# Kernel optimization log

Measured on AMD Instinct MI355X. Metric: run time of the kernel, lower is better.

The kernel has to match this reference:

```python
import jax, jax.numpy as jnp
import numpy as np

N_NODES, N_EDGES = 100000, 1600000
D_IN, D_H, D_OUT = 256, 128, 32


def _gcn_conv(x, W, b, row, col, norm, n):
    # GCNConv: transform, normalized gather from source nodes, scatter-sum at targets, bias.
    h = x @ W                                   # [n, d_out]
    msgs = h[row] * norm[:, None]               # [E', d_out] edge messages
    out = jax.ops.segment_sum(msgs, col, num_segments=n)
    return out + b


def setup_inputs() -> dict:
    key = jax.random.key(0)
    k = jax.random.split(key, 6)
    x = jax.random.normal(k[0], (N_NODES, D_IN), dtype=jnp.float32)
    edge_index = jax.random.randint(k[1], (2, N_EDGES), 0, N_NODES, dtype=jnp.int64)
    # Glorot-ish scaled params (GCNConv lin has no bias; bias added post-aggregation)
    W1 = jax.random.normal(k[2], (D_IN, D_H), dtype=jnp.float32) * (1.0 / np.sqrt(D_IN))
    b1 = jnp.zeros((D_H,), dtype=jnp.float32)
    W2 = jax.random.normal(k[3], (D_H, D_OUT), dtype=jnp.float32) * (1.0 / np.sqrt(D_H))
    b2 = jnp.zeros((D_OUT,), dtype=jnp.float32)
    return {"x": x, "W1": W1, "b1": b1, "W2": W2, "b2": b2, "edge_index": edge_index}


def reference(x, W1, b1, W2, b2, edge_index):
    n = x.shape[0]
    loops = jnp.arange(n, dtype=edge_index.dtype)
    row = jnp.concatenate([edge_index[0], loops])   # sources (incl. self-loops)
    col = jnp.concatenate([edge_index[1], loops])   # targets
    # symmetric normalization deg^{-1/2} (deg >= 1 because of self-loops)
    deg = jax.ops.segment_sum(jnp.ones_like(col, dtype=x.dtype), col, num_segments=n)
    dinv = deg ** -0.5
    norm = dinv[row] * dinv[col]
    h = jax.nn.relu(_gcn_conv(x, W1, b1, row, col, norm, n))
    # F.dropout(training=False) is identity in eval mode
    out = _gcn_conv(h, W2, b2, row, col, norm, n)
    return jax.nn.log_softmax(out, axis=1)
```

## Files before the change

kernel.cpp:

```cpp
#include <hip/hip_runtime.h>
#include <math.h>

#define N_NODES 100000
#define N_EDGES 1600000
#define D_IN 256
#define D_H 128
#define D_OUT 32
#define N_PAD 102400
#define NB 196
#define CAPB 10240
#define CHUNK 4096

typedef long long ll;
typedef unsigned int uint;
typedef unsigned short ushort;
typedef unsigned char uchar;
typedef short frag_ab __attribute__((ext_vector_type(8)));
typedef float frag_cd __attribute__((ext_vector_type(4)));

__device__ __forceinline__ ushort f2bf(float f) {
    uint u = __float_as_uint(f);
    u += 0x7FFFu + ((u >> 16) & 1u);
    return (ushort)(u >> 16);
}
__device__ __forceinline__ float bfl(uint u) { return __uint_as_float(u << 16); }
__device__ __forceinline__ float bfh(uint u) { return __uint_as_float(u & 0xFFFF0000u); }
__device__ __forceinline__ uint packbf(float a, float b) {
    return (uint)f2bf(a) | ((uint)f2bf(b) << 16);
}

__global__ __launch_bounds__(256) void k_prep(const float* __restrict__ W1,
                                              const float* __restrict__ W2,
                                              ushort* __restrict__ w1t,
                                              ushort* __restrict__ w2t,
                                              int* __restrict__ gcur) {
    int gi = blockIdx.x * 256 + threadIdx.x;
    if (blockIdx.x == 0) gcur[threadIdx.x] = 0;
    if (gi < D_IN * D_H) {
        int k = gi >> 7, nn = gi & 127;
        w1t[nn * D_IN + k] = f2bf(W1[gi]);
    } else if (gi < D_IN * D_H + D_H * D_OUT) {
        int j = gi - D_IN * D_H;
        int k = j >> 5, nn = j & 31;
        w2t[nn * D_H + k] = f2bf(W2[j]);
    }
}

__global__ __launch_bounds__(256, 3) void k_fused(const int* __restrict__ row,
                                                  const int* __restrict__ col,
                                                  int* __restrict__ gcur,
                                                  uint* __restrict__ pairs,
                                                  const float* __restrict__ x,
                                                  const ushort* __restrict__ w1t,
                                                  ushort* __restrict__ hxs,
                                                  int n, int e) {
    __shared__ int cnt[NB];
    __shared__ int cur[NB];
    __shared__ int lstart[NB];
    const int t = threadIdx.x;
    const int GA = (e + CHUNK - 1) / CHUNK;
    const int bid = blockIdx.x;

    if (bid < GA) {
        if (t < NB) { cnt[t] = 0; cur[t] = 0; }
        __syncthreads();
        const int base = bid * CHUNK;
        const int end = min(base + CHUNK, e);
        int rs[16], cs[16];
#pragma unroll
        for (int j = 0; j < 16; j++) {
            int idx = base + t + j * 256;
            bool ok = idx < end;
            int c = ok ? col[idx] : 0;
            rs[j] = ok ? row[idx] : 0;
            cs[j] = ok ? c : -1;
            if (ok) atomicAdd(&cnt[c >> 9], 1);
        }
        __syncthreads();
        if (t < NB) {
            int v = cnt[t];
            lstart[t] = (v > 0) ? atomicAdd(&gcur[t], v) : 0;
        }
        __syncthreads();
#pragma unroll
        for (int j = 0; j < 16; j++) {
            int c = cs[j];
            if (c >= 0) {
                int b = c >> 9;
                int pos = lstart[b] + atomicAdd(&cur[b], 1);
                if (pos < CAPB)
                    pairs[b * CAPB + pos] = ((uint)rs[j] << 9) | (uint)(c & 511);
            }
        }
    } else {
        const int id = bid - GA;
        const int wv = t >> 6, lane = t & 63;
        const int lm = lane & 15, quad = lane >> 4;
        const int base = id * 128 + wv * 32;

        frag_cd acc[2][8];
#pragma unroll
        for (int mt = 0; mt < 2; mt++)
#pragma unroll
            for (int nt = 0; nt < 8; nt++) acc[mt][nt] = (frag_cd){0.f, 0.f, 0.f, 0.f};

        const float4* xr[2];
#pragma unroll
        for (int mt = 0; mt < 2; mt++) {
            int node = base + mt * 16 + lm;
            xr[mt] = (const float4*)(x + (ll)min(node, n - 1) * D_IN);
        }

#pragma unroll
        for (int ks = 0; ks < 8; ks++) {
            frag_ab a[2];
#pragma unroll
            for (int mt = 0; mt < 2; mt++) {
                float4 v0 = xr[mt][ks * 8 + quad * 2];
                float4 v1 = xr[mt][ks * 8 + quad * 2 + 1];
                uint* ap = (uint*)&a[mt];
                ap[0] = packbf(v0.x, v0.y);
                ap[1] = packbf(v0.z, v0.w);
                ap[2] = packbf(v1.x, v1.y);
                ap[3] = packbf(v1.z, v1.w);
            }
#pragma unroll
            for (int nt = 0; nt < 8; nt++) {
                frag_ab b = *(const frag_ab*)&w1t[(nt * 16 + lm) * D_IN + ks * 32 + quad * 8];
#pragma unroll
                for (int mt = 0; mt < 2; mt++)
                    acc[mt][nt] = __builtin_amdgcn_mfma_f32_16x16x32_bf16(
                        a[mt], b, acc[mt][nt], 0, 0, 0);
            }
        }

#pragma unroll
        for (int mt = 0; mt < 2; mt++) {
#pragma unroll
            for (int r = 0; r < 4; r++) {
                int node = base + mt * 16 + quad * 4 + r;
                if (node < n) {
#pragma unroll
                    for (int nt = 0; nt < 8; nt++)
                        hxs[(ll)node * D_H + nt * 16 + lm] = f2bf(acc[mt][nt][r]);
                }
            }
        }
    }
}

__global__ __launch_bounds__(512) void k_fillB(const uint* __restrict__ pairs,
                                               const int* __restrict__ gcur,
                                               int* __restrict__ deg,
                                               int* __restrict__ rp,
                                               float* __restrict__ dinv,
                                               int* __restrict__ csr_src, int n) {
    __shared__ int hcnt[512];
    __shared__ int cur[512];
    __shared__ int ssum[512];
    const int b = blockIdx.x, t = threadIdx.x;
    const int node0 = b << 9;
    hcnt[t] = 0;
    __syncthreads();
    const int cnt = min(gcur[b], CAPB);
    const uint* pr = pairs + b * CAPB;
    for (int i = t; i < cnt; i += 512) atomicAdd(&hcnt[pr[i] & 511], 1);
    __syncthreads();
    int d = hcnt[t];
    ssum[t] = d;
    __syncthreads();
    for (int o = 1; o < 512; o <<= 1) {
        int u2 = (t >= o) ? ssum[t - o] : 0;
        __syncthreads();
        ssum[t] += u2;
        __syncthreads();
    }
    int excl = ssum[t] - d;
    cur[t] = excl;
    {
        int vv = node0 + t;
        if (vv < n) {
            rp[vv] = b * CAPB + excl;
            deg[vv] = d;
            dinv[vv] = rsqrtf((float)(1 + d));
        }
    }
    __syncthreads();
    const int cbase = b * CAPB;
    for (int i = t; i < cnt; i += 512) {
        uint pp = pr[i];
        int pos = atomicAdd(&cur[pp & 511], 1);
        if (pos < CAPB) csr_src[cbase + pos] = (int)(pp >> 9);
    }
}

__global__ __launch_bounds__(256) void k_agg1(const uint* __restrict__ hxs,
                                              const int* __restrict__ csr_src,
                                              const int* __restrict__ rp,
                                              const int* __restrict__ deg,
                                              const float* __restrict__ dinv,
                                              const float* __restrict__ b1,
                                              uint* __restrict__ h, int n) {
    int v = blockIdx.x * 4 + (threadIdx.x >> 6);
    if (v >= n) return;
    int lane = threadIdx.x & 63;
    float dv = dinv[v];
    uint u = hxs[v * 64 + lane];
    float a0 = dv * bfl(u), a1 = dv * bfh(u);
    int s = rp[v], e = s + deg[v];
    int i = s;
    for (; i + 7 < e; i += 8) {
        int s0 = csr_src[i], s1 = csr_src[i + 1];
        int s2 = csr_src[i + 2], s3 = csr_src[i + 3];
        int s4 = csr_src[i + 4], s5 = csr_src[i + 5];
        int s6 = csr_src[i + 6], s7 = csr_src[i + 7];
        float n0 = dinv[s0], n1 = dinv[s1], n2 = dinv[s2], n3 = dinv[s3];
        float n4 = dinv[s4], n5 = dinv[s5], n6 = dinv[s6], n7 = dinv[s7];
        uint u0 = hxs[s0 * 64 + lane], u1 = hxs[s1 * 64 + lane];
        uint u2 = hxs[s2 * 64 + lane], u3 = hxs[s3 * 64 + lane];
        uint u4 = hxs[s4 * 64 + lane], u5 = hxs[s5 * 64 + lane];
        uint u6 = hxs[s6 * 64 + lane], u7 = hxs[s7 * 64 + lane];
        a0 = fmaf(n0, bfl(u0), a0); a0 = fmaf(n1, bfl(u1), a0);
        a0 = fmaf(n2, bfl(u2), a0); a0 = fmaf(n3, bfl(u3), a0);
        a0 = fmaf(n4, bfl(u4), a0); a0 = fmaf(n5, bfl(u5), a0);
        a0 = fmaf(n6, bfl(u6), a0); a0 = fmaf(n7, bfl(u7), a0);
        a1 = fmaf(n0, bfh(u0), a1); a1 = fmaf(n1, bfh(u1), a1);
        a1 = fmaf(n2, bfh(u2), a1); a1 = fmaf(n3, bfh(u3), a1);
        a1 = fmaf(n4, bfh(u4), a1); a1 = fmaf(n5, bfh(u5), a1);
        a1 = fmaf(n6, bfh(u6), a1); a1 = fmaf(n7, bfh(u7), a1);
    }
    for (; i + 1 < e; i += 2) {
        int s0 = csr_src[i], s1 = csr_src[i + 1];
        float n0 = dinv[s0], n1 = dinv[s1];
        uint u0 = hxs[s0 * 64 + lane], u1 = hxs[s1 * 64 + lane];
        a0 = fmaf(n0, bfl(u0), a0); a0 = fmaf(n1, bfl(u1), a0);
        a1 = fmaf(n0, bfh(u0), a1); a1 = fmaf(n1, bfh(u1), a1);
    }
    if (i < e) {
        int s0 = csr_src[i];
        float n0 = dinv[s0];
        uint u0 = hxs[s0 * 64 + lane];
        a0 = fmaf(n0, bfl(u0), a0);
        a1 = fmaf(n0, bfh(u0), a1);
    }
    float2 bb = ((const float2*)b1)[lane];
    h[v * 64 + lane] = packbf(fmaxf(fmaf(dv, a0, bb.x), 0.f),
                              fmaxf(fmaf(dv, a1, bb.y), 0.f));
}

__global__ __launch_bounds__(256) void k_gemm2(const ushort* __restrict__ h,
                                               const ushort* __restrict__ w2t,
                                               const float* __restrict__ dinv,
                                               ushort* __restrict__ hx2s, int n) {
    const int tid = threadIdx.x;
    const int wv = tid >> 6, lane = tid & 63;
    const int lm = lane & 15, quad = lane >> 4;
    const int base = blockIdx.x * 128 + wv * 32;

    frag_cd acc[2][2];
#pragma unroll
    for (int mt = 0; mt < 2; mt++)
#pragma unroll
        for (int nt = 0; nt < 2; nt++) acc[mt][nt] = (frag_cd){0.f, 0.f, 0.f, 0.f};

    const ushort* hr[2];
#pragma unroll
    for (int mt = 0; mt < 2; mt++) {
        int node = base + mt * 16 + lm;
        hr[mt] = h + (ll)min(node, n - 1) * D_H;
    }

#pragma unroll
    for (int ks = 0; ks < 4; ks++) {
        frag_ab a[2], b[2];
#pragma unroll
        for (int mt = 0; mt < 2; mt++)
            a[mt] = *(const frag_ab*)&hr[mt][ks * 32 + quad * 8];
#pragma unroll
        for (int nt = 0; nt < 2; nt++)
            b[nt] = *(const frag_ab*)&w2t[(nt * 16 + lm) * D_H + ks * 32 + quad * 8];
#pragma unroll
        for (int mt = 0; mt < 2; mt++)
#pragma unroll
            for (int nt = 0; nt < 2; nt++)
                acc[mt][nt] = __builtin_amdgcn_mfma_f32_16x16x32_bf16(
                    a[mt], b[nt], acc[mt][nt], 0, 0, 0);
    }

#pragma unroll
    for (int mt = 0; mt < 2; mt++) {
#pragma unroll
        for (int r = 0; r < 4; r++) {
            int node = base + mt * 16 + quad * 4 + r;
            if (node < n) {
                float dv = dinv[node];
#pragma unroll
                for (int nt = 0; nt < 2; nt++)
                    hx2s[(ll)node * D_OUT + nt * 16 + lm] = f2bf(acc[mt][nt][r] * dv);
            }
        }
    }
}

__global__ __launch_bounds__(256) void k_agg2(const uint* __restrict__ hx2s,
                                              const int* __restrict__ csr_src,
                                              const int* __restrict__ rp,
                                              const int* __restrict__ deg,
                                              const float* __restrict__ dinv,
                                              const float* __restrict__ b2,
                                              float2* __restrict__ out, int n) {
    int v = blockIdx.x * 16 + (threadIdx.x >> 4);
    if (v >= n) return;
    int l16 = threadIdx.x & 15;
    uint u = hx2s[v * 16 + l16];
    float a0 = bfl(u), a1 = bfh(u);
    int s = rp[v], e = s + deg[v];
    int i = s;
    for (; i + 7 < e; i += 8) {
        int s0 = csr_src[i], s1 = csr_src[i + 1];
        int s2 = csr_src[i + 2], s3 = csr_src[i + 3];
        int s4 = csr_src[i + 4], s5 = csr_src[i + 5];
        int s6 = csr_src[i + 6], s7 = csr_src[i + 7];
        uint u0 = hx2s[s0 * 16 + l16], u1 = hx2s[s1 * 16 + l16];
        uint u2 = hx2s[s2 * 16 + l16], u3 = hx2s[s3 * 16 + l16];
        uint u4 = hx2s[s4 * 16 + l16], u5 = hx2s[s5 * 16 + l16];
        uint u6 = hx2s[s6 * 16 + l16], u7 = hx2s[s7 * 16 + l16];
        a0 += bfl(u0) + bfl(u1) + bfl(u2) + bfl(u3) + bfl(u4) + bfl(u5) + bfl(u6) + bfl(u7);
        a1 += bfh(u0) + bfh(u1) + bfh(u2) + bfh(u3) + bfh(u4) + bfh(u5) + bfh(u6) + bfh(u7);
    }
    for (; i + 1 < e; i += 2) {
        int s0 = csr_src[i], s1 = csr_src[i + 1];
        uint u0 = hx2s[s0 * 16 + l16], u1 = hx2s[s1 * 16 + l16];
        a0 += bfl(u0) + bfl(u1);
        a1 += bfh(u0) + bfh(u1);
    }
    if (i < e) {
        uint u0 = hx2s[csr_src[i] * 16 + l16];
        a0 += bfl(u0);
        a1 += bfh(u0);
    }
    float dv = dinv[v];
    float2 bb = ((const float2*)b2)[l16];
    float t0 = fmaf(dv, a0, bb.x), t1 = fmaf(dv, a1, bb.y);
    float mx = fmaxf(t0, t1);
#pragma unroll
    for (int m = 8; m >= 1; m >>= 1) mx = fmaxf(mx, __shfl_xor(mx, m));
    float sum = __expf(t0 - mx) + __expf(t1 - mx);
#pragma unroll
    for (int m = 8; m >= 1; m >>= 1) sum += __shfl_xor(sum, m);
    float lse = mx + __logf(sum);
    out[v * 16 + l16] = make_float2(t0 - lse, t1 - lse);
}

extern "C" void kernel_launch(void* const* d_in, const int* in_sizes, int n_in,
                              void* d_out, int out_size, void* d_ws, size_t ws_size,
                              hipStream_t stream) {
    const float* x  = (const float*)d_in[0];
    const float* W1 = (const float*)d_in[1];
    const float* b1 = (const float*)d_in[2];
    const float* W2 = (const float*)d_in[3];
    const float* b2 = (const float*)d_in[4];
    const int*   ei = (const int*)d_in[5];
    const int* row = ei;
    const int* col = ei + N_EDGES;

    int*    ws_i    = (int*)d_ws;
    int*    deg     = ws_i;
    int*    gcur    = ws_i + N_PAD;
    int*    rp      = ws_i + N_PAD + 256;
    float*  dinv    = (float*)(ws_i + 2 * N_PAD + 256);
    int*    csr_src = ws_i + 3 * N_PAD + 256;
    uint*   pairs   = (uint*)(csr_src + NB * CAPB);
    ushort* w1t     = (ushort*)(pairs + NB * CAPB);
    ushort* w2t     = w1t + D_IN * D_H;
    ushort* hxs     = w2t + D_H * D_OUT;
    ushort* h       = hxs + (ll)N_NODES * D_H;
    ushort* hx2s    = h + (ll)N_NODES * D_H;

    const int n = N_NODES, e = N_EDGES;

    k_prep<<<(D_IN * D_H + D_H * D_OUT + 255) / 256, 256, 0, stream>>>(W1, W2, w1t, w2t, gcur);

    const int GA = (e + CHUNK - 1) / CHUNK;
    const int GG = (n + 127) / 128;
    k_fused<<<GA + GG, 256, 0, stream>>>(row, col, gcur, pairs, x, w1t, hxs, n, e);

    k_fillB<<<NB, 512, 0, stream>>>(pairs, gcur, deg, rp, dinv, csr_src, n);
    k_agg1<<<(n + 3) / 4, 256, 0, stream>>>((const uint*)hxs, csr_src, rp, deg, dinv, b1,
                                            (uint*)h, n);
    k_gemm2<<<(n + 127) / 128, 256, 0, stream>>>(h, w2t, dinv, hx2s, n);
    k_agg2<<<(n + 15) / 16, 256, 0, stream>>>((const uint*)hx2s, csr_src, rp, deg, dinv, b2,
                                              (float2*)d_out, n);
}
```

Measured before the change: 339.2 us.

## Replace block-local bucket histogram with per-thread global sub-bucket atomics

Edge binning drops the shared-memory count/prefix/scatter passes with their three barriers. Each edge now does a global atomicAdd on one of 8 sub-counters per bucket (chosen by thread index) and writes into a fixed-capacity sub-slot. fillB iterates the 8 sub-slots per bucket. This trades barrier and shared-memory overhead for about 1.6M global atomics spread over 1568 counters. It also risks overflow, since each sub-slot holds only 1280 entries, and edge order within buckets becomes nondeterministic.

```diff
diff --git a/kernel.cpp b/kernel.cpp
--- a/kernel.cpp
+++ b/kernel.cpp
@@ -9,12 +9,13 @@
 #define N_PAD 102400
 #define NB 196
 #define CAPB 10240
+#define SUBCAP 1280
+#define NCUR (NB * 8)
 #define CHUNK 4096
 
 typedef long long ll;
 typedef unsigned int uint;
 typedef unsigned short ushort;
-typedef unsigned char uchar;
 typedef short frag_ab __attribute__((ext_vector_type(8)));
 typedef float frag_cd __attribute__((ext_vector_type(4)));
 
@@ -35,7 +36,7 @@
                                               ushort* __restrict__ w2t,
                                               int* __restrict__ gcur) {
     int gi = blockIdx.x * 256 + threadIdx.x;
-    if (blockIdx.x == 0) gcur[threadIdx.x] = 0;
+    if (gi < NCUR) gcur[gi] = 0;
     if (gi < D_IN * D_H) {
         int k = gi >> 7, nn = gi & 127;
         w1t[nn * D_IN + k] = f2bf(W1[gi]);
@@ -46,51 +47,28 @@
     }
 }
 
-__global__ __launch_bounds__(256, 3) void k_fused(const int* __restrict__ row,
-                                                  const int* __restrict__ col,
-                                                  int* __restrict__ gcur,
-                                                  uint* __restrict__ pairs,
-                                                  const float* __restrict__ x,
-                                                  const ushort* __restrict__ w1t,
-                                                  ushort* __restrict__ hxs,
-                                                  int n, int e) {
-    __shared__ int cnt[NB];
-    __shared__ int cur[NB];
-    __shared__ int lstart[NB];
+__global__ __launch_bounds__(256) void k_fused(const int* __restrict__ row,
+                                               const int* __restrict__ col,
+                                               int* __restrict__ gcur,
+                                               uint* __restrict__ pairs,
+                                               const float* __restrict__ x,
+                                               const ushort* __restrict__ w1t,
+                                               ushort* __restrict__ hxs,
+                                               int n, int e) {
     const int t = threadIdx.x;
     const int GA = (e + CHUNK - 1) / CHUNK;
     const int bid = blockIdx.x;
 
     if (bid < GA) {
-        if (t < NB) { cnt[t] = 0; cur[t] = 0; }
-        __syncthreads();
         const int base = bid * CHUNK;
         const int end = min(base + CHUNK, e);
-        int rs[16], cs[16];
-#pragma unroll
-        for (int j = 0; j < 16; j++) {
-            int idx = base + t + j * 256;
-            bool ok = idx < end;
-            int c = ok ? col[idx] : 0;
-            rs[j] = ok ? row[idx] : 0;
-            cs[j] = ok ? c : -1;
-            if (ok) atomicAdd(&cnt[c >> 9], 1);
-        }
-        __syncthreads();
-        if (t < NB) {
-            int v = cnt[t];
-            lstart[t] = (v > 0) ? atomicAdd(&gcur[t], v) : 0;
-        }
-        __syncthreads();
-#pragma unroll
-        for (int j = 0; j < 16; j++) {
-            int c = cs[j];
-            if (c >= 0) {
-                int b = c >> 9;
-                int pos = lstart[b] + atomicAdd(&cur[b], 1);
-                if (pos < CAPB)
-                    pairs[b * CAPB + pos] = ((uint)rs[j] << 9) | (uint)(c & 511);
-            }
+        const int s = t & 7;
+        for (int idx = base + t; idx < end; idx += 256) {
+            int c = col[idx], r = row[idx];
+            int b = c >> 9;
+            int pos = atomicAdd(&gcur[b * 8 + s], 1);
+            if (pos < SUBCAP)
+                pairs[b * CAPB + s * SUBCAP + pos] = ((uint)r << 9) | (uint)(c & 511);
         }
     } else {
         const int id = bid - GA;
@@ -162,9 +140,12 @@
     const int node0 = b << 9;
     hcnt[t] = 0;
     __syncthreads();
-    const int cnt = min(gcur[b], CAPB);
     const uint* pr = pairs + b * CAPB;
-    for (int i = t; i < cnt; i += 512) atomicAdd(&hcnt[pr[i] & 511], 1);
+#pragma unroll
+    for (int s = 0; s < 8; s++) {
+        int cnt = min(gcur[b * 8 + s], SUBCAP);
+        for (int i = t; i < cnt; i += 512) atomicAdd(&hcnt[pr[s * SUBCAP + i] & 511], 1);
+    }
     __syncthreads();
     int d = hcnt[t];
     ssum[t] = d;
@@ -187,10 +168,14 @@
     }
     __syncthreads();
     const int cbase = b * CAPB;
-    for (int i = t; i < cnt; i += 512) {
-        uint pp = pr[i];
-        int pos = atomicAdd(&cur[pp & 511], 1);
-        if (pos < CAPB) csr_src[cbase + pos] = (int)(pp >> 9);
+#pragma unroll
+    for (int s = 0; s < 8; s++) {
+        int cnt = min(gcur[b * 8 + s], SUBCAP);
+        for (int i = t; i < cnt; i += 512) {
+            uint pp = pr[s * SUBCAP + i];
+            int pos = atomicAdd(&cur[pp & 511], 1);
+            if (pos < CAPB) csr_src[cbase + pos] = (int)(pp >> 9);
+        }
     }
 }
 
@@ -367,9 +352,9 @@
     int*    ws_i    = (int*)d_ws;
     int*    deg     = ws_i;
     int*    gcur    = ws_i + N_PAD;
-    int*    rp      = ws_i + N_PAD + 256;
-    float*  dinv    = (float*)(ws_i + 2 * N_PAD + 256);
-    int*    csr_src = ws_i + 3 * N_PAD + 256;
+    int*    rp      = ws_i + N_PAD + 2048;
+    float*  dinv    = (float*)(ws_i + 2 * N_PAD + 2048);
+    int*    csr_src = ws_i + 3 * N_PAD + 2048;
     uint*   pairs   = (uint*)(csr_src + NB * CAPB);
     ushort* w1t     = (ushort*)(pairs + NB * CAPB);
     ushort* w2t     = w1t + D_IN * D_H;
```

After: 521.6 us. 53.8% more time.
